# Kernel tuning notes

Hardware: AMD Instinct MI355X
Metric: run time of the kernel (lower is better)

Reference implementation:

```python
import jax, jax.numpy as jnp
import numpy as np

FS = 11      # filter_size per spatial dim
N_ITER = 5   # mean-field iterations


def _gaussian_kernel1d(inv_theta, spacing, fs):
    # distances scaled by per-sample spacing; center tap zeroed (message passing excludes self)
    d = spacing * jnp.arange(-(fs // 2), fs // 2 + 1, dtype=jnp.float32)
    k = jnp.exp(-(d * inv_theta) ** 2 / 2)
    return k * (1.0 - jax.nn.one_hot(fs // 2, fs, dtype=k.dtype))


def _conv1d_last(x, kernel):
    # valid cross-correlation along the last axis; kernel is symmetric so conv == corr
    xr = x.reshape(-1, 1, x.shape[-1])
    out = jax.lax.conv_general_dilated(xr, kernel.reshape(1, 1, -1), (1,), 'VALID')
    return out.reshape(*x.shape[:-1], out.shape[-1])


def _smooth_single(x, spacing, inv_theta):
    # x: (C, H, W) -> separable zero-center Gaussian filter, per-sample kernels
    p = FS // 2
    x = jnp.pad(x, ((0, 0), (p, p), (p, p)))
    kh = _gaussian_kernel1d(inv_theta[0], spacing[0], FS)
    kw = _gaussian_kernel1d(inv_theta[1], spacing[1], FS)
    x = _conv1d_last(jnp.swapaxes(x, 1, 2), kh)  # conv along H -> (C, W+2p, H)
    x = _conv1d_last(jnp.swapaxes(x, 1, 2), kw)  # conv along W -> (C, H, W)
    return x


def setup_inputs() -> dict:
    key = jax.random.key(0)
    k1, = jax.random.split(key, 1)
    x = jax.random.normal(k1, (8, 19, 512, 512), dtype=jnp.float32)
    spatial_spacings = jnp.ones((8, 2), dtype=jnp.float32)
    smoothness_weight = jnp.array(1.0, dtype=jnp.float32)
    inv_smoothness_theta = jnp.ones((2,), dtype=jnp.float32)  # 1 / smoothness_theta
    return {"x": x, "spatial_spacings": spatial_spacings,
            "smoothness_weight": smoothness_weight,
            "inv_smoothness_theta": inv_smoothness_theta}


def reference(x, spatial_spacings, smoothness_weight, inv_smoothness_theta):
    n_classes = x.shape[1]
    comp = -jnp.eye(n_classes, dtype=x.dtype)  # compatibility matrix -(l1 == l2)
    negative_unary = x
    smooth = jax.vmap(_smooth_single, in_axes=(0, 0, None))
    for _ in range(N_ITER):
        q = jax.nn.softmax(x, axis=1)
        m = smoothness_weight * smooth(q, spatial_spacings, inv_smoothness_theta)
        m = jnp.einsum('bchw,cd->bdhw', m, comp)
        x = negative_unary - m
    return x  # returns='logits'
```

## Files before the change

kernel.cpp:

```cpp
#include <hip/hip_runtime.h>

#define FS 11
#define HFS 5

constexpr int Bn = 8, Cn = 19, Hn = 512, Wn = 512;
constexpr int HWn = Hn * Wn;
constexpr int CHWn = Cn * HWn;
constexpr int TOTn = Bn * CHWn;

constexpr int TH = 32, TW = 64;
constexpr int HR  = TH + 10;
constexpr int HC4 = 20;
constexpr int NP4 = HR * HC4;
constexpr int QS  = 84;
constexpr int WSS = 68;

__device__ __forceinline__ float rfl(float x) {
    return __uint_as_float(__builtin_amdgcn_readfirstlane(__float_as_uint(x)));
}

__global__ void k_taps(const float* __restrict__ spacing,
                       const float* __restrict__ inv_theta,
                       const float* __restrict__ wgt,
                       float* __restrict__ taps) {
    int t = threadIdx.x;
    if (t < Bn * 2 * FS) {
        int j = t % FS;
        int dim = (t / FS) & 1;
        int b = t / (2 * FS);
        float d = spacing[b * 2 + dim] * (float)(j - HFS);
        float a = d * inv_theta[dim];
        float k = __expf(-0.5f * a * a);
        if (j == HFS) k = 0.0f;
        if (dim == 1) k *= wgt[0];
        taps[t] = k;
    }
}

__global__ __launch_bounds__(256, 4) void k_fused(const float* __restrict__ xin,
                                                  const float* __restrict__ x0,
                                                  float* __restrict__ xout,
                                                  const float* __restrict__ taps) {
    __shared__ float qs[HR * QS];
    __shared__ float ws[HR * WSS];

    const int tid = threadIdx.x;
    const int w0 = blockIdx.x * TW;
    const int h0 = blockIdx.y * TH;
    const int b  = blockIdx.z;

    const float* tp = taps + b * (2 * FS);
    float kh[FS], kw[FS];
#pragma unroll
    for (int j = 0; j < FS; j++) { kh[j] = rfl(tp[j]); kw[j] = rfl(tp[FS + j]); }

    const float* xb = xin + b * CHWn;

    int off[4], lo[4];
    bool act[4], it[4];
#pragma unroll
    for (int k = 0; k < 4; k++) {
        int i = tid + 256 * k;
        it[k] = (i < NP4);
        int r = i / HC4, c4 = i % HC4;
        int hh = h0 - 5 + r;
        int ww = w0 - 8 + 4 * c4;
        act[k] = it[k] && hh >= 0 && hh < Hn && ww >= 0 && ww <= Wn - 4;
        off[k] = hh * Wn + ww;
        lo[k]  = r * QS + 4 * c4;
    }

    float4 px[4], rinv[4];
    {
        float4 s[4];
#pragma unroll
        for (int k = 0; k < 4; k++) {
            s[k] = make_float4(0.f, 0.f, 0.f, 0.f);
            if (act[k]) {
                float4 v = *(const float4*)(xb + off[k]);
                px[k] = v;
                s[k].x = __expf(v.x); s[k].y = __expf(v.y);
                s[k].z = __expf(v.z); s[k].w = __expf(v.w);
            }
        }
#pragma unroll 2
        for (int c = 1; c < Cn; ++c) {
#pragma unroll
            for (int k = 0; k < 4; k++) {
                if (!act[k]) continue;
                float4 v = *(const float4*)(xb + c * HWn + off[k]);
                s[k].x += __expf(v.x); s[k].y += __expf(v.y);
                s[k].z += __expf(v.z); s[k].w += __expf(v.w);
            }
        }
#pragma unroll
        for (int k = 0; k < 4; k++)
            if (act[k])
                rinv[k] = make_float4(1.f / s[k].x, 1.f / s[k].y,
                                      1.f / s[k].z, 1.f / s[k].w);
    }

    const int t0  = 2 * (tid >> 4);
    const int col = 4 * (tid & 15);
    const int pix = (h0 + t0) * Wn + (w0 + col);

    for (int c = 0; c < Cn; ++c) {
#pragma unroll
        for (int k = 0; k < 4; k++) {
            if (!it[k]) continue;
            float4 qv = make_float4(0.f, 0.f, 0.f, 0.f);
            if (act[k]) {
                qv.x = __expf(px[k].x) * rinv[k].x;
                qv.y = __expf(px[k].y) * rinv[k].y;
                qv.z = __expf(px[k].z) * rinv[k].z;
                qv.w = __expf(px[k].w) * rinv[k].w;
            }
            *(float4*)&qs[lo[k]] = qv;
        }
        __syncthreads();

        if (c + 1 < Cn) {
#pragma unroll
            for (int k = 0; k < 4; k++)
                if (act[k]) px[k] = *(const float4*)(xb + (c + 1) * HWn + off[k]);
        }
        const int gi = (b * Cn + c) * HWn + pix;
        float4 xA = *(const float4*)(x0 + gi);
        float4 xB = *(const float4*)(x0 + gi + Wn);

#pragma unroll 1
        for (int i2 = tid; i2 < HR * 8; i2 += 256) {
            int r = i2 >> 3, g = i2 & 7;
            float t[24];
#pragma unroll
            for (int m = 0; m < 6; ++m)
                *(float4*)&t[4 * m] = *(const float4*)&qs[r * QS + 8 * g + 4 * m];
            float o[8];
#pragma unroll
            for (int k2 = 0; k2 < 8; ++k2) {
                float a = 0.f;
#pragma unroll
                for (int j = 0; j < FS; ++j) {
                    if (j == HFS) continue;
                    a = fmaf(kw[j], t[k2 + 3 + j], a);
                }
                o[k2] = a;
            }
            float4 oa = {o[0], o[1], o[2], o[3]};
            float4 ob = {o[4], o[5], o[6], o[7]};
            *(float4*)&ws[r * WSS + 8 * g]     = oa;
            *(float4*)&ws[r * WSS + 8 * g + 4] = ob;
        }
        __syncthreads();

        {
            float4 wv[12];
#pragma unroll
            for (int j = 0; j < 12; ++j)
                wv[j] = *(const float4*)&ws[(t0 + j) * WSS + col];
            float4 o0 = {0.f, 0.f, 0.f, 0.f}, o1 = {0.f, 0.f, 0.f, 0.f};
#pragma unroll
            for (int j = 0; j < FS; ++j) {
                if (j == HFS) continue;
                float kj = kh[j];
                o0.x = fmaf(kj, wv[j].x, o0.x);     o0.y = fmaf(kj, wv[j].y, o0.y);
                o0.z = fmaf(kj, wv[j].z, o0.z);     o0.w = fmaf(kj, wv[j].w, o0.w);
                o1.x = fmaf(kj, wv[j + 1].x, o1.x); o1.y = fmaf(kj, wv[j + 1].y, o1.y);
                o1.z = fmaf(kj, wv[j + 1].z, o1.z); o1.w = fmaf(kj, wv[j + 1].w, o1.w);
            }
            float4 ra = {xA.x + o0.x, xA.y + o0.y, xA.z + o0.z, xA.w + o0.w};
            float4 rb = {xB.x + o1.x, xB.y + o1.y, xB.z + o1.z, xB.w + o1.w};
            *(float4*)(xout + gi)      = ra;
            *(float4*)(xout + gi + Wn) = rb;
        }
    }
}

extern "C" void kernel_launch(void* const* d_in, const int* in_sizes, int n_in,
                              void* d_out, int out_size, void* d_ws, size_t ws_size,
                              hipStream_t stream) {
    const float* x0      = (const float*)d_in[0];
    const float* spacing = (const float*)d_in[1];
    const float* wgt     = (const float*)d_in[2];
    const float* itheta  = (const float*)d_in[3];
    float* out = (float*)d_out;

    float* A    = (float*)d_ws;
    float* taps = A + TOTn;

    k_taps<<<1, 256, 0, stream>>>(spacing, itheta, wgt, taps);

    dim3 g(Wn / TW, Hn / TH, Bn);

    k_fused<<<g, 256, 0, stream>>>(x0,  x0, out, taps);
    k_fused<<<g, 256, 0, stream>>>(out, x0, A,   taps);
    k_fused<<<g, 256, 0, stream>>>(A,   x0, out, taps);
    k_fused<<<g, 256, 0, stream>>>(out, x0, A,   taps);
    k_fused<<<g, 256, 0, stream>>>(A,   x0, out, taps);
}
```

Measured before the change: 899.2 us.

## Halve tile height, remap blocks across XCDs, raise occupancy to six blocks

Tile height drops from 32 to 16 rows. Each thread now does one horizontal-pass task and one output row instead of two, and the per-thread halo load slots fall from 4 to 3. The launch moves to a 1D grid whose block IDs are swizzled so that neighbouring tiles of the same batch land on the same XCD, and launch bounds allow 6 blocks per CU. The aim is more occupancy and better L2 locality, paid for by a larger halo fraction (26 rows loaded for 16 outputs), which means more redundant softmax exp work and more global reads per output.

Measured after the change: 1.038 ms. 15.4% more time.

```diff
diff --git a/kernel.cpp b/kernel.cpp
--- a/kernel.cpp
+++ b/kernel.cpp
@@ -8,12 +8,13 @@
 constexpr int CHWn = Cn * HWn;
 constexpr int TOTn = Bn * CHWn;
 
-constexpr int TH = 32, TW = 64;
+constexpr int TH = 16, TW = 64;
 constexpr int HR  = TH + 10;
 constexpr int HC4 = 20;
 constexpr int NP4 = HR * HC4;
 constexpr int QS  = 84;
 constexpr int WSS = 68;
+constexpr int NTASK = HR * 8;
 
 __device__ __forceinline__ float rfl(float x) {
     return __uint_as_float(__builtin_amdgcn_readfirstlane(__float_as_uint(x)));
@@ -37,7 +38,7 @@
     }
 }
 
-__global__ __launch_bounds__(256, 4) void k_fused(const float* __restrict__ xin,
+__global__ __launch_bounds__(256, 6) void k_fused(const float* __restrict__ xin,
                                                   const float* __restrict__ x0,
                                                   float* __restrict__ xout,
                                                   const float* __restrict__ taps) {
@@ -45,9 +46,12 @@
     __shared__ float ws[HR * WSS];
 
     const int tid = threadIdx.x;
-    const int w0 = blockIdx.x * TW;
-    const int h0 = blockIdx.y * TH;
-    const int b  = blockIdx.z;
+    const int id = blockIdx.x;
+    const int fl = (id & 7) * 256 + (id >> 3);
+    const int b  = fl >> 8;
+    const int t8 = fl & 255;
+    const int h0 = (t8 >> 3) * TH;
+    const int w0 = (t8 & 7) * TW;
 
     const float* tp = taps + b * (2 * FS);
     float kh[FS], kw[FS];
@@ -56,10 +60,10 @@
 
     const float* xb = xin + b * CHWn;
 
-    int off[4], lo[4];
-    bool act[4], it[4];
-#pragma unroll
-    for (int k = 0; k < 4; k++) {
+    int off[3], lo[3];
+    bool it[3], act[3];
+#pragma unroll
+    for (int k = 0; k < 3; k++) {
         int i = tid + 256 * k;
         it[k] = (i < NP4);
         int r = i / HC4, c4 = i % HC4;
@@ -70,11 +74,11 @@
         lo[k]  = r * QS + 4 * c4;
     }
 
-    float4 px[4], rinv[4];
+    float4 px[3], rinv[3];
     {
-        float4 s[4];
-#pragma unroll
-        for (int k = 0; k < 4; k++) {
+        float4 s[3];
+#pragma unroll
+        for (int k = 0; k < 3; k++) {
             s[k] = make_float4(0.f, 0.f, 0.f, 0.f);
             if (act[k]) {
                 float4 v = *(const float4*)(xb + off[k]);
@@ -86,7 +90,7 @@
 #pragma unroll 2
         for (int c = 1; c < Cn; ++c) {
 #pragma unroll
-            for (int k = 0; k < 4; k++) {
+            for (int k = 0; k < 3; k++) {
                 if (!act[k]) continue;
                 float4 v = *(const float4*)(xb + c * HWn + off[k]);
                 s[k].x += __expf(v.x); s[k].y += __expf(v.y);
@@ -94,19 +98,27 @@
             }
         }
 #pragma unroll
-        for (int k = 0; k < 4; k++)
+        for (int k = 0; k < 3; k++)
             if (act[k])
                 rinv[k] = make_float4(1.f / s[k].x, 1.f / s[k].y,
                                       1.f / s[k].z, 1.f / s[k].w);
     }
 
-    const int t0  = 2 * (tid >> 4);
-    const int col = 4 * (tid & 15);
-    const int pix = (h0 + t0) * Wn + (w0 + col);
-
+    const bool wact = tid < NTASK;
+    const int wr = tid % HR;
+    const int wg = tid / HR;
+    const int qrd = wr * QS  + 8 * wg;
+    const int wwr = wr * WSS + 8 * wg;
+
+    const int rs  = tid >> 4;
+    const int cg  = tid & 15;
+    const int bws = rs * WSS + 4 * cg;
+    const int pix = (h0 + rs) * Wn + (w0 + 4 * cg);
+
+#pragma unroll 1
     for (int c = 0; c < Cn; ++c) {
 #pragma unroll
-        for (int k = 0; k < 4; k++) {
+        for (int k = 0; k < 3; k++) {
             if (!it[k]) continue;
             float4 qv = make_float4(0.f, 0.f, 0.f, 0.f);
             if (act[k]) {
@@ -121,20 +133,17 @@
 
         if (c + 1 < Cn) {
 #pragma unroll
-            for (int k = 0; k < 4; k++)
+            for (int k = 0; k < 3; k++)
                 if (act[k]) px[k] = *(const float4*)(xb + (c + 1) * HWn + off[k]);
         }
         const int gi = (b * Cn + c) * HWn + pix;
-        float4 xA = *(const float4*)(x0 + gi);
-        float4 xB = *(const float4*)(x0 + gi + Wn);
-
-#pragma unroll 1
-        for (int i2 = tid; i2 < HR * 8; i2 += 256) {
-            int r = i2 >> 3, g = i2 & 7;
+        const float4 xA = *(const float4*)(x0 + gi);
+
+        if (wact) {
             float t[24];
 #pragma unroll
             for (int m = 0; m < 6; ++m)
-                *(float4*)&t[4 * m] = *(const float4*)&qs[r * QS + 8 * g + 4 * m];
+                *(float4*)&t[4 * m] = *(const float4*)&qs[qrd + 4 * m];
             float o[8];
 #pragma unroll
             for (int k2 = 0; k2 < 8; ++k2) {
@@ -148,30 +157,23 @@
             }
             float4 oa = {o[0], o[1], o[2], o[3]};
             float4 ob = {o[4], o[5], o[6], o[7]};
-            *(float4*)&ws[r * WSS + 8 * g]     = oa;
-            *(float4*)&ws[r * WSS + 8 * g + 4] = ob;
+            *(float4*)&ws[wwr]     = oa;
+            *(float4*)&ws[wwr + 4] = ob;
         }
         __syncthreads();
 
         {
-            float4 wv[12];
-#pragma unroll
-            for (int j = 0; j < 12; ++j)
-                wv[j] = *(const float4*)&ws[(t0 + j) * WSS + col];
-            float4 o0 = {0.f, 0.f, 0.f, 0.f}, o1 = {0.f, 0.f, 0.f, 0.f};
+            float4 o = {0.f, 0.f, 0.f, 0.f};
 #pragma unroll
             for (int j = 0; j < FS; ++j) {
                 if (j == HFS) continue;
+                float4 v = *(const float4*)&ws[bws + j * WSS];
                 float kj = kh[j];
-                o0.x = fmaf(kj, wv[j].x, o0.x);     o0.y = fmaf(kj, wv[j].y, o0.y);
-                o0.z = fmaf(kj, wv[j].z, o0.z);     o0.w = fmaf(kj, wv[j].w, o0.w);
-                o1.x = fmaf(kj, wv[j + 1].x, o1.x); o1.y = fmaf(kj, wv[j + 1].y, o1.y);
-                o1.z = fmaf(kj, wv[j + 1].z, o1.z); o1.w = fmaf(kj, wv[j + 1].w, o1.w);
-            }
-            float4 ra = {xA.x + o0.x, xA.y + o0.y, xA.z + o0.z, xA.w + o0.w};
-            float4 rb = {xB.x + o1.x, xB.y + o1.y, xB.z + o1.z, xB.w + o1.w};
-            *(float4*)(xout + gi)      = ra;
-            *(float4*)(xout + gi + Wn) = rb;
+                o.x = fmaf(kj, v.x, o.x); o.y = fmaf(kj, v.y, o.y);
+                o.z = fmaf(kj, v.z, o.z); o.w = fmaf(kj, v.w, o.w);
+            }
+            float4 ra = {xA.x + o.x, xA.y + o.y, xA.z + o.z, xA.w + o.w};
+            *(float4*)(xout + gi) = ra;
         }
     }
 }
@@ -190,11 +192,9 @@
 
     k_taps<<<1, 256, 0, stream>>>(spacing, itheta, wgt, taps);
 
-    dim3 g(Wn / TW, Hn / TH, Bn);
-
-    k_fused<<<g, 256, 0, stream>>>(x0,  x0, out, taps);
-    k_fused<<<g, 256, 0, stream>>>(out, x0, A,   taps);
-    k_fused<<<g, 256, 0, stream>>>(A,   x0, out, taps);
-    k_fused<<<g, 256, 0, stream>>>(out, x0, A,   taps);
-    k_fused<<<g, 256, 0, stream>>>(A,   x0, out, taps);
-}
+    k_fused<<<2048, 256, 0, stream>>>(x0,  x0, out, taps);
+    k_fused<<<2048, 256, 0, stream>>>(out, x0, A,   taps);
+    k_fused<<<2048, 256, 0, stream>>>(A,   x0, out, taps);
+    k_fused<<<2048, 256, 0, stream>>>(out, x0, A,   taps);
+    k_fused<<<2048, 256, 0, stream>>>(A,   x0, out, taps);
+}
```
